# Kernel optimization log

Measured on AMD Instinct MI355X. Metric: run time of the kernel, lower is better.

## Reference

```python
import jax, jax.numpy as jnp
import numpy as np
from jax import lax
from math import sqrt

STYLE_DIM = 512
K = 3


def _equal_linear(latent, w, b):
    # EqualLinear: runtime weight scaling by 1/sqrt(fan_in)
    scale = 1.0 / sqrt(latent.shape[1])
    return latent @ (w.T * scale) + b


def _pixel_norm(x, axis=1, eps=1e-8):
    return x * jax.lax.rsqrt(jnp.mean(x * x, axis=axis, keepdims=True) + eps)


def _modconv(x, latent, weight, bias, el_w, el_b):
    # weight: (nc2, nc1, 3, 3); x: (B, nc1, H, W); latent: (B, style_dim)
    b = x.shape[0]
    nc2, nc1, k, _ = weight.shape
    fan_in = nc1 * k * k
    w = weight * sqrt(2.0 / fan_in)                      # (nc2, nc1, 3, 3)
    # style: s = 1 + PixelNorm(EqualLinear(latent))      # (B, nc1)
    s = 1.0 + _pixel_norm(_equal_linear(latent, el_w, el_b), axis=1)
    # demod: d_bo = rsqrt(sum_{c,k} (s_bc * w_ock)^2 + 1e-5)
    wsq = jnp.sum(w * w, axis=(2, 3))                    # (nc2, nc1)
    d = jax.lax.rsqrt(jnp.einsum('bc,oc->bo', s * s, wsq) + 1e-5)  # (B, nc2)
    # conv(x, s*w)*d  ==  conv(s*x, w)*d  (s is per input channel)
    xm = x * s[:, :, None, None]
    y = lax.conv_general_dilated(
        xm, w, window_strides=(1, 1), padding=[(1, 1), (1, 1)],
        dimension_numbers=('NCHW', 'OIHW', 'NCHW'))
    return y * d[:, :, None, None] + bias


def _style_block(x, latent, w0, b0, el0_w, el0_b, w1, b1, el1_w, el1_b):
    act_gain = sqrt(2.0)
    out = _modconv(x, latent, w0, b0, el0_w, el0_b)
    out = jax.nn.leaky_relu(out, 0.2) * act_gain
    out = _pixel_norm(out, axis=1)
    out = _modconv(out, latent, w1, b1, el1_w, el1_b)
    out = jax.nn.leaky_relu(out, 0.2) * act_gain
    out = _pixel_norm(out, axis=1)
    return out


def setup_inputs() -> dict:
    key = jax.random.key(0)
    ks = jax.random.split(key, 8)
    B, NC1, NC2, H, W = 8, 256, 256, 128, 128
    return {
        'x': jax.random.normal(ks[0], (B, NC1, H, W), jnp.float32),
        'latent': jax.random.normal(ks[1], (B, STYLE_DIM), jnp.float32),
        'w0': jax.random.normal(ks[2], (NC2, NC1, K, K), jnp.float32),
        'b0': jnp.zeros((1, NC2, 1, 1), jnp.float32),
        'el0_w': jax.random.normal(ks[3], (NC1, STYLE_DIM), jnp.float32),
        'el0_b': jnp.zeros((NC1,), jnp.float32),
        'w1': jax.random.normal(ks[4], (NC2, NC2, K, K), jnp.float32),
        'b1': jnp.zeros((1, NC2, 1, 1), jnp.float32),
        'el1_w': jax.random.normal(ks[5], (NC2, STYLE_DIM), jnp.float32),
        'el1_b': jnp.zeros((NC2,), jnp.float32),
    }


def reference(x, latent, w0, b0, el0_w, el0_b, w1, b1, el1_w, el1_b):
    return _style_block(x, latent, w0, b0, el0_w, el0_b, w1, b1, el1_w, el1_b)
```

## Files before the change

### kernel.cpp

```cpp
#include <hip/hip_runtime.h>
#include <hip/hip_bf16.h>

typedef __attribute__((ext_vector_type(8))) short short8;
typedef __attribute__((ext_vector_type(16))) float f32x16;

typedef const __attribute__((address_space(1))) unsigned int* gas1_t;
typedef __attribute__((address_space(3))) unsigned int* las3_t;

__device__ __forceinline__ unsigned short f2bf(float x) {
    unsigned int u = __float_as_uint(x);
    u = (u + 0x7fffu + ((u >> 16) & 1u)) >> 16;
    return (unsigned short)u;
}

__device__ __forceinline__ int4 pack8(const unsigned short* u) {
    int4 p;
    p.x = (int)((unsigned)u[0] | ((unsigned)u[1] << 16));
    p.y = (int)((unsigned)u[2] | ((unsigned)u[3] << 16));
    p.z = (int)((unsigned)u[4] | ((unsigned)u[5] << 16));
    p.w = (int)((unsigned)u[6] | ((unsigned)u[7] << 16));
    return p;
}

__device__ __forceinline__ void gld_lds16(const void* g, void* l) {
    __builtin_amdgcn_global_load_lds((gas1_t)g, (las3_t)l, 16, 0, 0);
}

__global__ void style_kernel(const float* __restrict__ latent,
                             const float* __restrict__ elw0, const float* __restrict__ elb0,
                             const float* __restrict__ elw1, const float* __restrict__ elb1,
                             float* __restrict__ s_arr) {
    const int cv = blockIdx.x >> 3;
    const int b  = blockIdx.x & 7;
    const int c  = threadIdx.x;
    const float* elw = cv ? elw1 : elw0;
    const float* elb = cv ? elb1 : elb0;

    __shared__ float lat[512];
    lat[c] = latent[b * 512 + c];
    lat[c + 256] = latent[b * 512 + c + 256];
    __syncthreads();

    float accv = 0.f;
    const float* wrow = elw + (size_t)c * 512;
#pragma unroll 8
    for (int k = 0; k < 512; ++k) accv += lat[k] * wrow[k];
    const float lin = accv * 0.04419417382415922f + elb[c];

    float sq = lin * lin;
#pragma unroll
    for (int off = 32; off >= 1; off >>= 1) sq += __shfl_xor(sq, off);
    __shared__ float wsum[4];
    if ((threadIdx.x & 63) == 0) wsum[threadIdx.x >> 6] = sq;
    __syncthreads();
    const float total = wsum[0] + wsum[1] + wsum[2] + wsum[3];
    const float s = 1.0f + lin * rsqrtf(total * (1.0f / 256.0f) + 1e-8f);
    s_arr[(cv * 8 + b) * 256 + c] = s;
}

__global__ void wsq_kernel(const float* __restrict__ w0, const float* __restrict__ w1,
                           float* __restrict__ wsq) {
    const int cv = blockIdx.x >> 8;
    const int o  = blockIdx.x & 255;
    const int c  = threadIdx.x;
    const float* w = cv ? w1 : w0;
    const size_t base = ((size_t)o * 256 + c) * 9;
    float ssum = 0.f;
#pragma unroll
    for (int t = 0; t < 9; ++t) { float v = w[base + t]; ssum += v * v; }
    wsq[((size_t)cv * 256 + o) * 256 + c] = ssum * (2.0f / 2304.0f);
}

__global__ void demod_kernel(const float* __restrict__ s_arr, const float* __restrict__ wsq,
                             float* __restrict__ d_arr) {
    const int cv = blockIdx.x >> 3;
    const int b  = blockIdx.x & 7;
    const int o  = threadIdx.x;
    __shared__ float ss[256];
    float sv = s_arr[(cv * 8 + b) * 256 + o];
    ss[o] = sv * sv;
    __syncthreads();
    const float* wrow = wsq + ((size_t)cv * 256 + o) * 256;
    float accv = 0.f;
#pragma unroll 8
    for (int c = 0; c < 256; ++c) accv += ss[c] * wrow[c];
    d_arr[(cv * 8 + b) * 256 + o] = rsqrtf(accv + 1e-5f);
}

__global__ void fold_kernel(const float* __restrict__ w0, const float* __restrict__ w1,
                            const float* __restrict__ s_arr, const float* __restrict__ d_arr,
                            unsigned short* __restrict__ wm0, unsigned short* __restrict__ wm1) {
    const int cv = blockIdx.y;
    const int e  = blockIdx.x * 256 + threadIdx.x;
    const float* w = cv ? w1 : w0;
    unsigned short* wm = cv ? wm1 : wm0;
    const int slab = e >> 13;
    const int idx  = e & 8191;
    const int b  = slab / 72;
    const int s2 = slab - b * 72;
    const int cc = s2 / 9;
    const int t  = s2 - cc * 9;
    const int o  = idx >> 5;
    const int c5 = idx & 31;
    const int c  = cc * 32 + c5;
    const float val = w[((size_t)o * 256 + c) * 9 + t] * 0.029462782549439483f
                    * s_arr[(cv * 8 + b) * 256 + c] * d_arr[(cv * 8 + b) * 256 + o];
    wm[((size_t)slab << 13) + (c5 >> 3) * 2048 + o * 8 + (c5 & 7)] = f2bf(val);
}

__global__ void convert_kernel(const float* __restrict__ x, unsigned short* __restrict__ xq) {
    const int blk = blockIdx.x;
    const int hh  = blk & 127;
    const int bg_ = blk >> 7;
    const int g   = bg_ & 31;
    const int b   = bg_ >> 5;
    __shared__ float sx[8][128];
    const int tid = threadIdx.x;
#pragma unroll
    for (int i = 0; i < 4; ++i) {
        const int idx = tid + i * 256;
        const int c8 = idx >> 7, p = idx & 127;
        sx[c8][p] = x[(((size_t)b * 256 + g * 8 + c8) * 128 + hh) * 128 + p];
    }
    __syncthreads();
    if (tid < 128) {
        const int p = tid;
        unsigned short u[8];
#pragma unroll
        for (int j = 0; j < 8; ++j) u[j] = f2bf(sx[j][p]);
        *(int4*)(xq + ((((size_t)b * 32 + g) * 128 + hh) * 128 + p) * 8) = pack8(u);
    }
}

template<bool FINAL_OUT>
__global__ __launch_bounds__(512, 2) void conv_kernel(
    const unsigned short* __restrict__ in_q, const unsigned short* __restrict__ wmod,
    const float* __restrict__ bias, const unsigned short* __restrict__ zpg,
    void* __restrict__ out_v) {

    __shared__ __align__(16) char lds[136256];

    const int tid  = threadIdx.x;
    const int b    = blockIdx.x & 7;
    const int rp   = blockIdx.x >> 3;
    const int h0   = rp * 2;
    const int lane = tid & 63;
    const int wr   = tid >> 6;
    const int wm   = wr & 3;
    const int wn   = wr >> 2;
    const int l31  = lane & 31;
    const int khg  = lane >> 5;

    float* sbias = (float*)(lds + 131136);
    if (tid < 256) sbias[tid] = bias[tid];
    if (tid < 4)   *(int4*)(lds + 131072 + tid * 16) = (int4){0, 0, 0, 0};

    int aoff[2][2];
#pragma unroll
    for (int mb = 0; mb < 2; ++mb)
#pragma unroll
        for (int kh = 0; kh < 2; ++kh)
            aoff[mb][kh] = ((khg + 2 * kh) * 256 + wm * 64 + mb * 32 + l31) * 16;

    const unsigned short* wmb = wmod + (size_t)b * 589824;
    const unsigned short* xqb = in_q + (size_t)b * 4194304;

    auto issueA3 = [&](const char* src, int nbuf) {
        char* db = lds + nbuf * 49152 + wr * 2048;
        const char* s = src + wr * 2048 + lane * 16;
#pragma unroll
        for (int j = 0; j < 3; ++j) {
            gld_lds16(s + j * 16384,        db + j * 16384);
            gld_lds16(s + j * 16384 + 1024, db + j * 16384 + 1024);
        }
    };

    auto issueBrows = [&](int cc, int r0, int r1) {
        const int koct = tid >> 7;
        const int px   = tid & 127;
#pragma unroll
        for (int r = 0; r < 4; ++r) {
            if (r < r0 || r >= r1) continue;
            const int hin = h0 - 1 + r;
            const unsigned short* src = ((unsigned)hin < 128u)
                ? xqb + (((size_t)(cc * 4 + koct) * 128 + hin) * 128 + px) * 8
                : zpg;
            gld_lds16(src, lds + 98304 + r * 8192 + koct * 2048 + (wr & 1) * 1024);
        }
    };

    f32x16 acc[2][4];
#pragma unroll
    for (int mb = 0; mb < 2; ++mb)
#pragma unroll
        for (int nb = 0; nb < 4; ++nb)
#pragma unroll
            for (int r = 0; r < 16; ++r) acc[mb][nb][r] = 0.f;

    issueA3((const char*)wmb, 0);
    issueBrows(0, 0, 4);
    __syncthreads();

    const char* gA = (const char*)wmb + 49152;
#pragma unroll 1
    for (int cc = 0; cc < 8; ++cc) {
#pragma unroll
        for (int r = 0; r < 3; ++r) {
            const int g = cc * 3 + r;
            if (r == 0 && cc > 0) issueBrows(cc, 2, 4);
            if (r == 2 && cc < 7) issueBrows(cc + 1, 0, 2);
            if (g < 23) { issueA3(gA, (g + 1) & 1); gA += 49152; }
            const char* Ac = lds + (g & 1) * 49152;
#pragma unroll
            for (int i = 0; i < 3; ++i) {
                short8 af[2][2], bf[4][2];
#pragma unroll
                for (int mb = 0; mb < 2; ++mb)
#pragma unroll
                    for (int kh = 0; kh < 2; ++kh)
                        af[mb][kh] = *(const short8*)(Ac + i * 16384 + aoff[mb][kh]);
#pragma unroll
                for (int nb = 0; nb < 4; ++nb)
#pragma unroll
                    for (int kh = 0; kh < 2; ++kh) {
                        int off = 98304 + (wn + r) * 8192 + (khg + 2 * kh) * 2048
                                + (nb * 32 + l31 + i - 1) * 16;
                        if (i == 0 && nb == 0) off = (l31 == 0)  ? 131072 : off;
                        if (i == 2 && nb == 3) off = (l31 == 31) ? 131072 : off;
                        bf[nb][kh] = *(const short8*)(lds + off);
                    }
#pragma unroll
                for (int kh = 0; kh < 2; ++kh)
#pragma unroll
                    for (int mb = 0; mb < 2; ++mb)
#pragma unroll
                        for (int nb = 0; nb < 4; ++nb)
                            acc[mb][nb] = __builtin_amdgcn_mfma_f32_32x32x16_bf16(
                                af[mb][kh], bf[nb][kh], acc[mb][nb], 0, 0, 0);
            }
            asm volatile("s_waitcnt vmcnt(0) lgkmcnt(0)" ::: "memory");
            __builtin_amdgcn_sched_barrier(0);
            __builtin_amdgcn_s_barrier();
        }
    }

    float psum[4] = {0.f, 0.f, 0.f, 0.f};
    const float actGain = 1.4142135623730951f;
#pragma unroll
    for (int mb = 0; mb < 2; ++mb)
#pragma unroll
        for (int rg = 0; rg < 16; ++rg) {
            const int row = (rg & 3) + 8 * (rg >> 2) + 4 * khg;
            const float bo = sbias[wm * 64 + mb * 32 + row];
#pragma unroll
            for (int nb = 0; nb < 4; ++nb) {
                float v = acc[mb][nb][rg] + bo;
                v = (v > 0.f ? v : 0.2f * v) * actGain;
                acc[mb][nb][rg] = v;
                psum[nb] += v * v;
            }
        }
#pragma unroll
    for (int nb = 0; nb < 4; ++nb) psum[nb] += __shfl_xor(psum[nb], 32);
    float* red = (float*)(lds + 132160);
    if (lane < 32) {
#pragma unroll
        for (int nb = 0; nb < 4; ++nb)
            red[(wn * 4 + wm) * 128 + nb * 32 + l31] = psum[nb];
    }
    __syncthreads();
    float rs[4];
#pragma unroll
    for (int nb = 0; nb < 4; ++nb) {
        const int p = nb * 32 + l31;
        const float ssum = red[(wn * 4 + 0) * 128 + p] + red[(wn * 4 + 1) * 128 + p]
                         + red[(wn * 4 + 2) * 128 + p] + red[(wn * 4 + 3) * 128 + p];
        rs[nb] = rsqrtf(ssum * (1.0f / 256.0f) + 1e-8f);
    }

    const int h = h0 + wn;
    if (FINAL_OUT) {
        float* outF = (float*)out_v;
#pragma unroll
        for (int mb = 0; mb < 2; ++mb)
#pragma unroll
            for (int rg = 0; rg < 16; ++rg) {
                const int row = (rg & 3) + 8 * (rg >> 2) + 4 * khg;
                const int o = wm * 64 + mb * 32 + row;
                const size_t rb = (((size_t)b * 256 + o) * 128 + h) * 128;
#pragma unroll
                for (int nb = 0; nb < 4; ++nb)
                    outF[rb + nb * 32 + l31] = acc[mb][nb][rg] * rs[nb];
            }
    } else {
        unsigned short* outB = (unsigned short*)out_v;
        char* wreg = lds + wr * 8192;
#pragma unroll
        for (int mb = 0; mb < 2; ++mb) {
#pragma unroll
            for (int rg = 0; rg < 16; rg += 2) {
                const int row = (rg & 3) + 8 * (rg >> 2) + 4 * khg;
#pragma unroll
                for (int nb = 0; nb < 4; ++nb) {
                    const int pxl = nb * 32 + l31;
                    const unsigned lo = f2bf(acc[mb][nb][rg]     * rs[nb]);
                    const unsigned hi = f2bf(acc[mb][nb][rg + 1] * rs[nb]);
                    *(unsigned int*)(wreg + pxl * 64 + (((row >> 3) ^ (pxl & 3)) << 4)
                                     + (row & 7) * 2) = lo | (hi << 16);
                }
            }
            asm volatile("s_waitcnt lgkmcnt(0)" ::: "memory");
#pragma unroll
            for (int oc = 0; oc < 4; ++oc)
#pragma unroll
                for (int ph = 0; ph < 2; ++ph) {
                    const int pxl = ph * 64 + lane;
                    const int4 v = *(const int4*)(wreg + pxl * 64 + ((oc ^ (pxl & 3)) << 4));
                    const int g = wm * 8 + mb * 4 + oc;
                    *(int4*)(outB + ((((size_t)b * 32 + g) * 128 + h) * 128 + pxl) * 8) = v;
                }
            asm volatile("s_waitcnt lgkmcnt(0)" ::: "memory");
        }
    }
}

extern "C" void kernel_launch(void* const* d_in, const int* in_sizes, int n_in,
                              void* d_out, int out_size, void* d_ws, size_t ws_size,
                              hipStream_t stream) {
    (void)in_sizes; (void)n_in; (void)out_size; (void)ws_size;
    const float* x      = (const float*)d_in[0];
    const float* latent = (const float*)d_in[1];
    const float* w0     = (const float*)d_in[2];
    const float* b0     = (const float*)d_in[3];
    const float* el0w   = (const float*)d_in[4];
    const float* el0b   = (const float*)d_in[5];
    const float* w1     = (const float*)d_in[6];
    const float* b1     = (const float*)d_in[7];
    const float* el1w   = (const float*)d_in[8];
    const float* el1b   = (const float*)d_in[9];

    char* ws = (char*)d_ws;
    float* s_arr = (float*)ws;
    float* d_arr = (float*)(ws + 16384);
    float* wsq   = (float*)(ws + 32768);
    unsigned short* zpg = (unsigned short*)(ws + 32768);
    unsigned short* wm0 = (unsigned short*)(ws + 557056);
    unsigned short* wm1 = (unsigned short*)(ws + 9994240);
    unsigned short* xq  = (unsigned short*)(ws + 19431424);
    unsigned short* tmp = (unsigned short*)(ws + 86540288);

    style_kernel<<<16, 256, 0, stream>>>(latent, el0w, el0b, el1w, el1b, s_arr);
    wsq_kernel<<<512, 256, 0, stream>>>(w0, w1, wsq);
    demod_kernel<<<16, 256, 0, stream>>>(s_arr, wsq, d_arr);
    hipMemsetAsync(zpg, 0, 256, stream);
    fold_kernel<<<dim3(18432, 2), 256, 0, stream>>>(w0, w1, s_arr, d_arr, wm0, wm1);
    convert_kernel<<<32768, 256, 0, stream>>>(x, xq);

    conv_kernel<false><<<512, 512, 0, stream>>>(xq, wm0, b0, zpg, tmp);
    conv_kernel<true><<<512, 512, 0, stream>>>(tmp, wm1, b1, zpg, d_out);
}
```

Before: 364.2 us.

## Double conv block to 1024 threads, splitting pixel columns across waves

Both conv kernels now launch 1024-thread blocks with 16 waves instead of 8. Each wave covers 64 of the 128 output pixels, so each wave holds half the accumulator state. The weight and input-row staging loads, the pixel-norm reduction slots and the epilogue writes are redistributed to match the new wave layout. The aim is more resident waves per CU to hide LDS and MFMA latency. The costs are less reuse of each A fragment, more LDS read traffic, and a tighter per-thread register budget under the new launch bounds, which may cause spills.

```diff
diff --git a/kernel.cpp b/kernel.cpp
--- a/kernel.cpp
+++ b/kernel.cpp
@@ -133,7 +133,7 @@
 }
 
 template<bool FINAL_OUT>
-__global__ __launch_bounds__(512, 2) void conv_kernel(
+__global__ __launch_bounds__(1024, 4) void conv_kernel(
     const unsigned short* __restrict__ in_q, const unsigned short* __restrict__ wmod,
     const float* __restrict__ bias, const unsigned short* __restrict__ zpg,
     void* __restrict__ out_v) {
@@ -147,7 +147,8 @@
     const int lane = tid & 63;
     const int wr   = tid >> 6;
     const int wm   = wr & 3;
-    const int wn   = wr >> 2;
+    const int wn2  = (wr >> 2) & 1;
+    const int wrow = wr >> 3;
     const int l31  = lane & 31;
     const int khg  = lane >> 5;
 
@@ -161,39 +162,49 @@
 #pragma unroll
         for (int kh = 0; kh < 2; ++kh)
             aoff[mb][kh] = ((khg + 2 * kh) * 256 + wm * 64 + mb * 32 + l31) * 16;
+    int boff[2][2];
+#pragma unroll
+    for (int nb = 0; nb < 2; ++nb)
+#pragma unroll
+        for (int kh = 0; kh < 2; ++kh)
+            boff[nb][kh] = 98304 + (khg + 2 * kh) * 2048
+                         + (wn2 * 64 + nb * 32 + l31) * 16;
+    const bool isL = (wn2 == 0) && (l31 == 0);
+    const bool isR = (wn2 == 1) && (l31 == 31);
 
     const unsigned short* wmb = wmod + (size_t)b * 589824;
     const unsigned short* xqb = in_q + (size_t)b * 4194304;
 
     auto issueA3 = [&](const char* src, int nbuf) {
-        char* db = lds + nbuf * 49152 + wr * 2048;
-        const char* s = src + wr * 2048 + lane * 16;
-#pragma unroll
-        for (int j = 0; j < 3; ++j) {
-            gld_lds16(s + j * 16384,        db + j * 16384);
-            gld_lds16(s + j * 16384 + 1024, db + j * 16384 + 1024);
+        char* db = lds + nbuf * 49152 + wr * 1024;
+        const char* s = src + wr * 1024 + lane * 16;
+#pragma unroll
+        for (int j = 0; j < 3; ++j)
+            gld_lds16(s + j * 16384, db + j * 16384);
+    };
+
+    auto issueBrows = [&](int cc, int r0, int r1) {
+        const int row = wr >> 2;
+        if (row < r0 || row >= r1) return;
+        const int koct = wr & 3;
+        char* dst = lds + 98304 + row * 8192 + koct * 2048;
+        const int hin = h0 - 1 + row;
+        if ((unsigned)hin < 128u) {
+            const unsigned short* src = xqb
+                + ((size_t)(cc * 4 + koct) * 128 + hin) * 1024 + lane * 8;
+            gld_lds16(src,       dst);
+            gld_lds16(src + 512, dst + 1024);
+        } else {
+            gld_lds16(zpg, dst);
+            gld_lds16(zpg, dst + 1024);
         }
     };
 
-    auto issueBrows = [&](int cc, int r0, int r1) {
-        const int koct = tid >> 7;
-        const int px   = tid & 127;
-#pragma unroll
-        for (int r = 0; r < 4; ++r) {
-            if (r < r0 || r >= r1) continue;
-            const int hin = h0 - 1 + r;
-            const unsigned short* src = ((unsigned)hin < 128u)
-                ? xqb + (((size_t)(cc * 4 + koct) * 128 + hin) * 128 + px) * 8
-                : zpg;
-            gld_lds16(src, lds + 98304 + r * 8192 + koct * 2048 + (wr & 1) * 1024);
-        }
-    };
-
-    f32x16 acc[2][4];
+    f32x16 acc[2][2];
 #pragma unroll
     for (int mb = 0; mb < 2; ++mb)
 #pragma unroll
-        for (int nb = 0; nb < 4; ++nb)
+        for (int nb = 0; nb < 2; ++nb)
 #pragma unroll
             for (int r = 0; r < 16; ++r) acc[mb][nb][r] = 0.f;
 
@@ -213,20 +224,20 @@
             const char* Ac = lds + (g & 1) * 49152;
 #pragma unroll
             for (int i = 0; i < 3; ++i) {
-                short8 af[2][2], bf[4][2];
+                short8 af[2][2], bf[2][2];
 #pragma unroll
                 for (int mb = 0; mb < 2; ++mb)
 #pragma unroll
                     for (int kh = 0; kh < 2; ++kh)
                         af[mb][kh] = *(const short8*)(Ac + i * 16384 + aoff[mb][kh]);
-#pragma unroll
-                for (int nb = 0; nb < 4; ++nb)
+                const int badd = (wrow + r) * 8192 + (i - 1) * 16;
+#pragma unroll
+                for (int nb = 0; nb < 2; ++nb)
 #pragma unroll
                     for (int kh = 0; kh < 2; ++kh) {
-                        int off = 98304 + (wn + r) * 8192 + (khg + 2 * kh) * 2048
-                                + (nb * 32 + l31 + i - 1) * 16;
-                        if (i == 0 && nb == 0) off = (l31 == 0)  ? 131072 : off;
-                        if (i == 2 && nb == 3) off = (l31 == 31) ? 131072 : off;
+                        int off = boff[nb][kh] + badd;
+                        if (i == 0 && nb == 0) off = isL ? 131072 : off;
+                        if (i == 2 && nb == 1) off = isR ? 131072 : off;
                         bf[nb][kh] = *(const short8*)(lds + off);
                     }
 #pragma unroll
@@ -234,7 +245,7 @@
 #pragma unroll
                     for (int mb = 0; mb < 2; ++mb)
 #pragma unroll
-                        for (int nb = 0; nb < 4; ++nb)
+                        for (int nb = 0; nb < 2; ++nb)
                             acc[mb][nb] = __builtin_amdgcn_mfma_f32_32x32x16_bf16(
                                 af[mb][kh], bf[nb][kh], acc[mb][nb], 0, 0, 0);
             }
@@ -244,7 +255,7 @@
         }
     }
 
-    float psum[4] = {0.f, 0.f, 0.f, 0.f};
+    float psum[2] = {0.f, 0.f};
     const float actGain = 1.4142135623730951f;
 #pragma unroll
     for (int mb = 0; mb < 2; ++mb)
@@ -253,32 +264,33 @@
             const int row = (rg & 3) + 8 * (rg >> 2) + 4 * khg;
             const float bo = sbias[wm * 64 + mb * 32 + row];
 #pragma unroll
-            for (int nb = 0; nb < 4; ++nb) {
+            for (int nb = 0; nb < 2; ++nb) {
                 float v = acc[mb][nb][rg] + bo;
                 v = (v > 0.f ? v : 0.2f * v) * actGain;
                 acc[mb][nb][rg] = v;
                 psum[nb] += v * v;
             }
         }
-#pragma unroll
-    for (int nb = 0; nb < 4; ++nb) psum[nb] += __shfl_xor(psum[nb], 32);
+    psum[0] += __shfl_xor(psum[0], 32);
+    psum[1] += __shfl_xor(psum[1], 32);
     float* red = (float*)(lds + 132160);
+    const int rslot = (wrow * 2 + wn2) * 4 + wm;
     if (lane < 32) {
-#pragma unroll
-        for (int nb = 0; nb < 4; ++nb)
-            red[(wn * 4 + wm) * 128 + nb * 32 + l31] = psum[nb];
-    }
-    __syncthreads();
-    float rs[4];
-#pragma unroll
-    for (int nb = 0; nb < 4; ++nb) {
+        red[rslot * 64 + l31]      = psum[0];
+        red[rslot * 64 + 32 + l31] = psum[1];
+    }
+    __syncthreads();
+    float rs[2];
+#pragma unroll
+    for (int nb = 0; nb < 2; ++nb) {
         const int p = nb * 32 + l31;
-        const float ssum = red[(wn * 4 + 0) * 128 + p] + red[(wn * 4 + 1) * 128 + p]
-                         + red[(wn * 4 + 2) * 128 + p] + red[(wn * 4 + 3) * 128 + p];
+        const int base = (wrow * 2 + wn2) * 4;
+        const float ssum = red[(base + 0) * 64 + p] + red[(base + 1) * 64 + p]
+                         + red[(base + 2) * 64 + p] + red[(base + 3) * 64 + p];
         rs[nb] = rsqrtf(ssum * (1.0f / 256.0f) + 1e-8f);
     }
 
-    const int h = h0 + wn;
+    const int h = h0 + wrow;
     if (FINAL_OUT) {
         float* outF = (float*)out_v;
 #pragma unroll
@@ -287,21 +299,21 @@
             for (int rg = 0; rg < 16; ++rg) {
                 const int row = (rg & 3) + 8 * (rg >> 2) + 4 * khg;
                 const int o = wm * 64 + mb * 32 + row;
-                const size_t rb = (((size_t)b * 256 + o) * 128 + h) * 128;
-#pragma unroll
-                for (int nb = 0; nb < 4; ++nb)
+                const size_t rb = (((size_t)b * 256 + o) * 128 + h) * 128 + wn2 * 64;
+#pragma unroll
+                for (int nb = 0; nb < 2; ++nb)
                     outF[rb + nb * 32 + l31] = acc[mb][nb][rg] * rs[nb];
             }
     } else {
         unsigned short* outB = (unsigned short*)out_v;
-        char* wreg = lds + wr * 8192;
+        char* wreg = lds + wr * 4096;
 #pragma unroll
         for (int mb = 0; mb < 2; ++mb) {
 #pragma unroll
             for (int rg = 0; rg < 16; rg += 2) {
                 const int row = (rg & 3) + 8 * (rg >> 2) + 4 * khg;
 #pragma unroll
-                for (int nb = 0; nb < 4; ++nb) {
+                for (int nb = 0; nb < 2; ++nb) {
                     const int pxl = nb * 32 + l31;
                     const unsigned lo = f2bf(acc[mb][nb][rg]     * rs[nb]);
                     const unsigned hi = f2bf(acc[mb][nb][rg + 1] * rs[nb]);
@@ -311,14 +323,13 @@
             }
             asm volatile("s_waitcnt lgkmcnt(0)" ::: "memory");
 #pragma unroll
-            for (int oc = 0; oc < 4; ++oc)
-#pragma unroll
-                for (int ph = 0; ph < 2; ++ph) {
-                    const int pxl = ph * 64 + lane;
-                    const int4 v = *(const int4*)(wreg + pxl * 64 + ((oc ^ (pxl & 3)) << 4));
-                    const int g = wm * 8 + mb * 4 + oc;
-                    *(int4*)(outB + ((((size_t)b * 32 + g) * 128 + h) * 128 + pxl) * 8) = v;
-                }
+            for (int oc = 0; oc < 4; ++oc) {
+                const int pxl = lane;
+                const int4 v = *(const int4*)(wreg + pxl * 64 + ((oc ^ (pxl & 3)) << 4));
+                const int gch = wm * 8 + mb * 4 + oc;
+                *(int4*)(outB + ((((size_t)b * 32 + gch) * 128 + h) * 128
+                                 + wn2 * 64 + pxl) * 8) = v;
+            }
             asm volatile("s_waitcnt lgkmcnt(0)" ::: "memory");
         }
     }
@@ -356,6 +367,6 @@
     fold_kernel<<<dim3(18432, 2), 256, 0, stream>>>(w0, w1, s_arr, d_arr, wm0, wm1);
     convert_kernel<<<32768, 256, 0, stream>>>(x, xq);
 
-    conv_kernel<false><<<512, 512, 0, stream>>>(xq, wm0, b0, zpg, tmp);
-    conv_kernel<true><<<512, 512, 0, stream>>>(tmp, wm1, b1, zpg, d_out);
-}
+    conv_kernel<false><<<512, 1024, 0, stream>>>(xq, wm0, b0, zpg, tmp);
+    conv_kernel<true><<<512, 1024, 0, stream>>>(tmp, wm1, b1, zpg, d_out);
+}
```

Result: no change. 370.7 us (+1.8%).
